# Performance work log

Measured on AMD Instinct MI355X. Metric: run time of the kernel, lower is better.

Reference implementation:

```python
import jax, jax.numpy as jnp
import numpy as np

S, B, E, H = 2048, 2, 1024, 16
DH = E // H
SCALING = DH ** -0.5


def setup_inputs() -> dict:
    key = jax.random.key(0)
    ks = jax.random.split(key, 9)
    std = 1.0 / np.sqrt(E)
    return {
        "query": jax.random.normal(ks[0], (S, B, E), jnp.float32),
        "wq": jax.random.normal(ks[1], (E, E), jnp.float32) * std,
        "bq": jax.random.normal(ks[2], (E,), jnp.float32) * 0.02,
        "wk": jax.random.normal(ks[3], (E, E), jnp.float32) * std,
        "bk": jax.random.normal(ks[4], (E,), jnp.float32) * 0.02,
        "wv": jax.random.normal(ks[5], (E, E), jnp.float32) * std,
        "bv": jax.random.normal(ks[6], (E,), jnp.float32) * 0.02,
        "wo": jax.random.normal(ks[7], (E, E), jnp.float32) * std,
        "bo": jax.random.normal(ks[8], (E,), jnp.float32) * 0.02,
    }


def reference(query, wq, bq, wk, bk, wv, bv, wo, bo):
    # query: [S, B, E] (time, batch, channel), self-attention: key=value=query
    q = (query @ wq.T + bq) * SCALING          # fairseq scales q, not scores
    k = query @ wk.T + bk
    v = query @ wv.T + bv
    # split heads: [S, B, H, DH]
    q = q.reshape(S, B, H, DH)
    k = k.reshape(S, B, H, DH)
    v = v.reshape(S, B, H, DH)
    scores = jnp.einsum("qbhd,kbhd->bhqk", q, k)   # [B, H, S, S]
    probs = jax.nn.softmax(scores, axis=-1)
    ctx = jnp.einsum("bhqk,kbhd->qbhd", probs, v)  # [S, B, H, DH]
    ctx = ctx.reshape(S, B, E)
    return ctx @ wo.T + bo                          # [S, B, E]
```

## Files before the change

### kernel.cpp

```cpp
#include <hip/hip_runtime.h>
#include <hip/hip_bf16.h>
#include <stdint.h>

#define S_LEN 2048
#define BATCH 2
#define EMB   1024
#define NH    16
#define DHEAD 64
#define ROWS  (S_LEN*BATCH)
#define SCALE_Q 0.18033688011112042f
#define DEFER_THR 11.0f

typedef __attribute__((ext_vector_type(8))) short bf16x8;
typedef __attribute__((ext_vector_type(4))) float f32x4;
typedef __attribute__((ext_vector_type(16))) float f32x16;

typedef const __attribute__((address_space(1))) void* gas_ptr;
typedef __attribute__((address_space(3))) void* las_ptr;
#define GLD16(g, l) __builtin_amdgcn_global_load_lds((gas_ptr)(g), (las_ptr)(l), 16, 0, 0)

__device__ __forceinline__ unsigned short f2b(float f) {
  union { float f; unsigned int u; } v; v.f = f;
  unsigned int u = v.u;
  unsigned int r = (u + 0x7FFFu + ((u >> 16) & 1u)) >> 16;
  return (unsigned short)r;
}

__device__ __forceinline__ unsigned cvt_pk_bf16(float lo, float hi) {
  unsigned r;
  asm("v_cvt_pk_bf16_f32 %0, %1, %2" : "=v"(r) : "v"(lo), "v"(hi));
  return r;
}

__device__ __forceinline__ float exp2_raw(float x) {
  float r;
  asm("v_exp_f32 %0, %1" : "=v"(r) : "v"(x));
  return r;
}

__device__ __forceinline__ void cvt8(const float* __restrict__ s,
                                     unsigned short* __restrict__ d, size_t i) {
  float4 a = *reinterpret_cast<const float4*>(s + i);
  float4 b = *reinterpret_cast<const float4*>(s + i + 4);
  uint4 o;
  o.x = (unsigned)f2b(a.x) | ((unsigned)f2b(a.y) << 16);
  o.y = (unsigned)f2b(a.z) | ((unsigned)f2b(a.w) << 16);
  o.z = (unsigned)f2b(b.x) | ((unsigned)f2b(b.y) << 16);
  o.w = (unsigned)f2b(b.z) | ((unsigned)f2b(b.w) << 16);
  *reinterpret_cast<uint4*>(d + i) = o;
}

__global__ __launch_bounds__(256) void cvt_all_kernel(
    const float* __restrict__ query,
    const float* __restrict__ wq, const float* __restrict__ wk,
    const float* __restrict__ wv, const float* __restrict__ wo,
    unsigned short* __restrict__ Xbf,
    unsigned short* __restrict__ Wqb, unsigned short* __restrict__ Wkb,
    unsigned short* __restrict__ Wvb, unsigned short* __restrict__ Wob) {
  int id = blockIdx.x;
  const float* s; unsigned short* d; size_t off;
  if (id < 2048) { s = query; d = Xbf; off = (size_t)id * 2048; }
  else {
    int wsel = (id - 2048) >> 9;
    off = (size_t)((id - 2048) & 511) * 2048;
    switch (wsel) {
      case 0:  s = wq; d = Wqb; break;
      case 1:  s = wk; d = Wkb; break;
      case 2:  s = wv; d = Wvb; break;
      default: s = wo; d = Wob; break;
    }
  }
  cvt8(s, d, off + (size_t)threadIdx.x * 8);
}

__device__ __forceinline__ void gemm_mainloop(const unsigned short* __restrict__ A,
                                              const unsigned short* __restrict__ Bw,
                                              int m0, int n0, f32x4 acc[4][4],
                                              unsigned short* Ab, unsigned short* Bb) {
  const int t    = threadIdx.x;
  const int lane = t & 63;
  const int w    = t >> 6;
  const int wr   = w >> 1, wc = w & 1;
  const int lm   = lane & 15;
  const int lq   = lane >> 4;

  f32x4 zf = {0.0f, 0.0f, 0.0f, 0.0f};
#pragma unroll
  for (int i = 0; i < 4; ++i)
#pragma unroll
    for (int j = 0; j < 4; ++j) acc[i][j] = zf;

  for (int k0 = 0; k0 < EMB; k0 += 64) {
#pragma unroll
    for (int q = 0; q < 4; ++q) {
      int c = t + q * 256;
      int r = c >> 3, ci = c & 7;
      int lc = ci ^ (r & 7);
      GLD16(A  + (size_t)(m0 + r) * EMB + k0 + lc * 8,
            (char*)Ab + (size_t)(q * 256 + w * 64) * 16);
      GLD16(Bw + (size_t)(n0 + r) * EMB + k0 + lc * 8,
            (char*)Bb + (size_t)(q * 256 + w * 64) * 16);
    }
    asm volatile("s_waitcnt vmcnt(0)" ::: "memory");
    __syncthreads();

#pragma unroll
    for (int kk = 0; kk < 2; ++kk) {
      bf16x8 af[4], bfr[4];
#pragma unroll
      for (int i = 0; i < 4; ++i) {
        int ra = wr * 64 + i * 16 + lm;
        af[i] = *reinterpret_cast<const bf16x8*>(
            &Ab[ra * 64 + ((kk * 4 + lq) ^ (ra & 7)) * 8]);
      }
#pragma unroll
      for (int j = 0; j < 4; ++j) {
        int rb = wc * 64 + j * 16 + lm;
        bfr[j] = *reinterpret_cast<const bf16x8*>(
            &Bb[rb * 64 + ((kk * 4 + lq) ^ (rb & 7)) * 8]);
      }
#pragma unroll
      for (int i = 0; i < 4; ++i)
#pragma unroll
        for (int j = 0; j < 4; ++j)
          acc[i][j] = __builtin_amdgcn_mfma_f32_16x16x32_bf16(af[i], bfr[j], acc[i][j], 0, 0, 0);
    }
    __syncthreads();
  }
}

__global__ __launch_bounds__(256) void gemm_qkv_kernel(
    const unsigned short* __restrict__ X,
    const unsigned short* __restrict__ Wq, const unsigned short* __restrict__ Wk,
    const unsigned short* __restrict__ Wv,
    const float* __restrict__ bq, const float* __restrict__ bk, const float* __restrict__ bv,
    unsigned short* __restrict__ Qb, unsigned short* __restrict__ Kb,
    unsigned short* __restrict__ Vtg) {
  __shared__ unsigned short SH[2][128 * 64];
  const int m0 = blockIdx.x * 128;
  const int n0 = blockIdx.y * 128;
  const int z  = blockIdx.z;
  const unsigned short* Bw = (z == 0) ? Wq : (z == 1) ? Wk : Wv;
  const float* bias        = (z == 0) ? bq : (z == 1) ? bk : bv;

  f32x4 acc[4][4];
  gemm_mainloop(X, Bw, m0, n0, acc, SH[0], SH[1]);

  const int t    = threadIdx.x;
  const int lane = t & 63;
  const int w    = t >> 6;
  const int wr   = w >> 1, wc = w & 1;
  const int lm   = lane & 15, lq = lane >> 4;

  if (z != 2) {
    unsigned short* Out = (z == 0) ? Qb : Kb;
    const float scale   = (z == 0) ? SCALE_Q : 1.0f;
#pragma unroll
    for (int j = 0; j < 4; ++j) {
      int col = n0 + wc * 64 + j * 16 + lm;
      int h = col >> 6, dd = col & 63;
      float bc = bias[col];
#pragma unroll
      for (int i = 0; i < 4; ++i) {
#pragma unroll
        for (int r = 0; r < 4; ++r) {
          int row = m0 + wr * 64 + i * 16 + lq * 4 + r;
          int s = row >> 1, b = row & 1;
          float v = (acc[i][j][r] + bc) * scale;
          Out[((size_t)(b * NH + h) * S_LEN + s) * DHEAD + dd] = f2b(v);
        }
      }
    }
  } else {
    unsigned short* T = &SH[0][0];
#pragma unroll
    for (int j = 0; j < 4; ++j) {
      int col = wc * 64 + j * 16 + lm;
      float bc = bias[n0 + col];
#pragma unroll
      for (int i = 0; i < 4; ++i) {
#pragma unroll
        for (int r = 0; r < 4; ++r) {
          int row = wr * 64 + i * 16 + lq * 4 + r;
          int idx = (row & 1) * 64 + (row >> 1);
          int chunk = idx >> 3, within = idx & 7;
          int pchunk = (chunk & 8) | ((chunk ^ col) & 7);
          T[col * 128 + pchunk * 8 + within] = f2b(acc[i][j][r] + bc);
        }
      }
    }
    __syncthreads();
#pragma unroll
    for (int itr = 0; itr < 8; ++itr) {
      int u = (t >> 3) + itr * 32;
      int col = u & 127, b = u >> 7;
      int c3 = t & 7;
      int pchunk = (b * 8) | ((c3 ^ col) & 7);
      bf16x8 vv = *reinterpret_cast<const bf16x8*>(&T[col * 128 + pchunk * 8]);
      int h = (n0 + col) >> 6, dd = (n0 + col) & 63;
      unsigned short* dst =
          Vtg + ((size_t)(b * NH + h) * DHEAD + dd) * S_LEN + (m0 >> 1);
      int p1 = ((c3 >> 1) << 4) | ((c3 & 1) << 2);
      union { bf16x8 v; uint4 u4; } cv; cv.v = vv;
      *reinterpret_cast<uint2*>(dst + p1)     = make_uint2(cv.u4.x, cv.u4.y);
      *reinterpret_cast<uint2*>(dst + p1 + 8) = make_uint2(cv.u4.z, cv.u4.w);
    }
  }
}

__global__ __launch_bounds__(256) void gemm_out_kernel(
    const unsigned short* __restrict__ Ctx, const unsigned short* __restrict__ Wo,
    const float* __restrict__ bo, float* __restrict__ Out) {
  __shared__ unsigned short Ab[64 * 64];
  __shared__ unsigned short Bb[128 * 64];
  const int m0 = blockIdx.x * 64;
  const int n0 = blockIdx.y * 128;
  const int t    = threadIdx.x;
  const int lane = t & 63;
  const int w    = t >> 6;
  const int wr   = w >> 1, wc = w & 1;
  const int lm   = lane & 15, lq = lane >> 4;

  f32x4 zf = {0.0f, 0.0f, 0.0f, 0.0f};
  f32x4 acc[2][4];
#pragma unroll
  for (int i = 0; i < 2; ++i)
#pragma unroll
    for (int j = 0; j < 4; ++j) acc[i][j] = zf;

  for (int k0 = 0; k0 < EMB; k0 += 64) {
#pragma unroll
    for (int q = 0; q < 2; ++q) {
      int c = t + q * 256;
      int r = c >> 3, ci = c & 7;
      int lc = ci ^ (r & 7);
      GLD16(Ctx + (size_t)(m0 + r) * EMB + k0 + lc * 8,
            (char*)Ab + (size_t)(q * 256 + w * 64) * 16);
    }
#pragma unroll
    for (int q = 0; q < 4; ++q) {
      int c = t + q * 256;
      int r = c >> 3, ci = c & 7;
      int lc = ci ^ (r & 7);
      GLD16(Wo + (size_t)(n0 + r) * EMB + k0 + lc * 8,
            (char*)Bb + (size_t)(q * 256 + w * 64) * 16);
    }
    asm volatile("s_waitcnt vmcnt(0)" ::: "memory");
    __syncthreads();

#pragma unroll
    for (int kk = 0; kk < 2; ++kk) {
      bf16x8 af[2], bfr[4];
#pragma unroll
      for (int i = 0; i < 2; ++i) {
        int ra = wr * 32 + i * 16 + lm;
        af[i] = *reinterpret_cast<const bf16x8*>(
            &Ab[ra * 64 + ((kk * 4 + lq) ^ (ra & 7)) * 8]);
      }
#pragma unroll
      for (int j = 0; j < 4; ++j) {
        int rb = wc * 64 + j * 16 + lm;
        bfr[j] = *reinterpret_cast<const bf16x8*>(
            &Bb[rb * 64 + ((kk * 4 + lq) ^ (rb & 7)) * 8]);
      }
#pragma unroll
      for (int i = 0; i < 2; ++i)
#pragma unroll
        for (int j = 0; j < 4; ++j)
          acc[i][j] = __builtin_amdgcn_mfma_f32_16x16x32_bf16(af[i], bfr[j], acc[i][j], 0, 0, 0);
    }
    __syncthreads();
  }

#pragma unroll
  for (int j = 0; j < 4; ++j) {
    int col = n0 + wc * 64 + j * 16 + lm;
    float bc = bo[col];
#pragma unroll
    for (int i = 0; i < 2; ++i) {
#pragma unroll
      for (int r = 0; r < 4; ++r) {
        int row = m0 + wr * 32 + i * 16 + lq * 4 + r;
        Out[(size_t)row * EMB + col] = acc[i][j][r] + bc;
      }
    }
  }
}

__global__ __launch_bounds__(256, 2) void attn_kernel(
    const unsigned short* __restrict__ Qb, const unsigned short* __restrict__ Kb,
    const unsigned short* __restrict__ Vtg, unsigned short* __restrict__ Ctx) {
  const int bh = blockIdx.x;
  const int q0 = blockIdx.y * 128;
  const int t    = threadIdx.x;
  const int lane = t & 63;
  const int w    = t >> 6;
  const int l31  = lane & 31;
  const int hh   = lane >> 5;
  const unsigned short* Q  = Qb  + (size_t)bh * S_LEN * DHEAD;
  const unsigned short* K  = Kb  + (size_t)bh * S_LEN * DHEAD;
  const unsigned short* Vt = Vtg + (size_t)bh * DHEAD * S_LEN;

  __shared__ unsigned short Kl[2][64 * 64];
  __shared__ unsigned short Vl[2][64 * 64];

  const int qw = q0 + w * 32;

  bf16x8 aq[4];
#pragma unroll
  for (int kk = 0; kk < 4; ++kk)
    aq[kk] = *reinterpret_cast<const bf16x8*>(
        Q + (size_t)(qw + l31) * DHEAD + kk * 16 + hh * 8);

  f32x16 z16 = {0.f,0.f,0.f,0.f, 0.f,0.f,0.f,0.f, 0.f,0.f,0.f,0.f, 0.f,0.f,0.f,0.f};
  f32x16 accO[2];
  accO[0] = z16; accO[1] = z16;
  float m_s = -1e30f, l_s = 0.0f;

  auto STAGE = [&](int b, int kb) {
#pragma unroll
    for (int q = 0; q < 2; ++q) {
      int c = t + q * 256;
      int r = c >> 3, p = c & 7;
      int lc = p ^ (r & 7);
      GLD16(K  + (size_t)(kb + r) * DHEAD + lc * 8,
            (char*)&Kl[b][0] + (size_t)(q * 256 + w * 64) * 16);
      GLD16(Vt + (size_t)r * S_LEN + kb + lc * 8,
            (char*)&Vl[b][0] + (size_t)(q * 256 + w * 64) * 16);
    }
  };

  const int NT = S_LEN / 64;
  STAGE(0, 0);
  STAGE(1, 64);

  for (int it = 0; it < NT; ++it) {
    const int cur = it & 1;
    if (it < NT - 1) {
      asm volatile("s_waitcnt vmcnt(4)" ::: "memory");
    } else {
      asm volatile("s_waitcnt vmcnt(0)" ::: "memory");
    }
    __builtin_amdgcn_s_barrier();

    f32x16 p32[2];
    __builtin_amdgcn_s_setprio(1);
#pragma unroll
    for (int ji = 0; ji < 2; ++ji) {
      f32x16 a = z16;
      int rr = ji * 32 + l31;
#pragma unroll
      for (int kk = 0; kk < 4; ++kk) {
        bf16x8 kf = *reinterpret_cast<const bf16x8*>(
            &Kl[cur][rr * 64 + ((kk * 2 + hh) ^ (rr & 7)) * 8]);
        a = __builtin_amdgcn_mfma_f32_32x32x16_bf16(kf, aq[kk], a, 0, 0, 0);
      }
      p32[ji] = a;
    }
    __builtin_amdgcn_s_setprio(0);

    float t8[8];
#pragma unroll
    for (int e = 0; e < 8; ++e)
      t8[e] = fmaxf(fmaxf(p32[0][e], p32[0][e + 8]),
                    fmaxf(p32[1][e], p32[1][e + 8]));
    float u0 = fmaxf(t8[0], t8[4]), u1 = fmaxf(t8[1], t8[5]);
    float u2 = fmaxf(t8[2], t8[6]), u3 = fmaxf(t8[3], t8[7]);
    float tm = fmaxf(fmaxf(u0, u1), fmaxf(u2, u3));
    tm = fmaxf(tm, __shfl_xor(tm, 32));

    if (!__all(tm - m_s <= DEFER_THR)) {
      float mn = fmaxf(m_s, tm);
      float sc = exp2_raw(m_s - mn);
      l_s *= sc;
      m_s = mn;
#pragma unroll
      for (int r = 0; r < 16; ++r) {
        float scr = __shfl(sc, (r & 3) + 8 * (r >> 2) + 4 * hh);
        accO[0][r] *= scr;
        accO[1][r] *= scr;
      }
    }

#pragma unroll
    for (int e = 0; e < 16; ++e) {
      p32[0][e] = exp2_raw(p32[0][e] - m_s);
      p32[1][e] = exp2_raw(p32[1][e] - m_s);
    }
    float s8[8];
#pragma unroll
    for (int e = 0; e < 8; ++e)
      s8[e] = (p32[0][e] + p32[0][e + 8]) + (p32[1][e] + p32[1][e + 8]);
    float v0 = (s8[0] + s8[4]) + (s8[1] + s8[5]);
    float v1 = (s8[2] + s8[6]) + (s8[3] + s8[7]);
    float ps = v0 + v1;
    ps += __shfl_xor(ps, 32);
    l_s += ps;

    bf16x8 pa[2][2];
#pragma unroll
    for (int ji = 0; ji < 2; ++ji) {
      uint4 lo4, hi4;
      lo4.x = cvt_pk_bf16(p32[ji][0],  p32[ji][1]);
      lo4.y = cvt_pk_bf16(p32[ji][2],  p32[ji][3]);
      lo4.z = cvt_pk_bf16(p32[ji][4],  p32[ji][5]);
      lo4.w = cvt_pk_bf16(p32[ji][6],  p32[ji][7]);
      hi4.x = cvt_pk_bf16(p32[ji][8],  p32[ji][9]);
      hi4.y = cvt_pk_bf16(p32[ji][10], p32[ji][11]);
      hi4.z = cvt_pk_bf16(p32[ji][12], p32[ji][13]);
      hi4.w = cvt_pk_bf16(p32[ji][14], p32[ji][15]);
      pa[ji][0] = *reinterpret_cast<bf16x8*>(&lo4);
      pa[ji][1] = *reinterpret_cast<bf16x8*>(&hi4);
    }

    __builtin_amdgcn_s_setprio(1);
#pragma unroll
    for (int ni = 0; ni < 2; ++ni) {
      int dd = ni * 32 + l31;
#pragma unroll
      for (int ji = 0; ji < 2; ++ji)
#pragma unroll
        for (int ss = 0; ss < 2; ++ss) {
          bf16x8 bv = *reinterpret_cast<const bf16x8*>(
              &Vl[cur][dd * 64 + ((ji * 4 + ss * 2 + hh) ^ (dd & 7)) * 8]);
          accO[ni] = __builtin_amdgcn_mfma_f32_32x32x16_bf16(pa[ji][ss], bv, accO[ni], 0, 0, 0);
        }
    }
    __builtin_amdgcn_s_setprio(0);

    asm volatile("s_waitcnt lgkmcnt(0)" ::: "memory");
    __builtin_amdgcn_sched_barrier(0);
    __builtin_amdgcn_s_barrier();

    if (it + 2 < NT) STAGE(cur, (it + 2) * 64);
  }

  const int b = bh >> 4, h = bh & 15;
#pragma unroll
  for (int r = 0; r < 16; ++r) {
    int row = (r & 3) + 8 * (r >> 2) + 4 * hh;
    float rl = 1.0f / __shfl(l_s, row);
    int srow = qw + row;
    size_t base = ((size_t)srow * BATCH + b) * EMB + (size_t)h * 64 + l31;
    Ctx[base]      = f2b(accO[0][r] * rl);
    Ctx[base + 32] = f2b(accO[1][r] * rl);
  }
}

extern "C" void kernel_launch(void* const* d_in, const int* in_sizes, int n_in,
                              void* d_out, int out_size, void* d_ws, size_t ws_size,
                              hipStream_t stream) {
  const float* query = (const float*)d_in[0];
  const float* wq = (const float*)d_in[1];
  const float* bq = (const float*)d_in[2];
  const float* wk = (const float*)d_in[3];
  const float* bk = (const float*)d_in[4];
  const float* wv = (const float*)d_in[5];
  const float* bv = (const float*)d_in[6];
  const float* wo = (const float*)d_in[7];
  const float* bo = (const float*)d_in[8];
  float* out = (float*)d_out;

  unsigned short* p = (unsigned short*)d_ws;
  unsigned short* Xbf = p;                        p += (size_t)ROWS * EMB;
  unsigned short* Wqb = p;                        p += (size_t)EMB * EMB;
  unsigned short* Wkb = p;                        p += (size_t)EMB * EMB;
  unsigned short* Wvb = p;                        p += (size_t)EMB * EMB;
  unsigned short* Wob = p;                        p += (size_t)EMB * EMB;
  unsigned short* Qb  = p;                        p += (size_t)ROWS * EMB;
  unsigned short* Kb  = p;                        p += (size_t)ROWS * EMB;
  unsigned short* Vtg = p;                        p += (size_t)ROWS * EMB;
  unsigned short* Ctx = p;                        p += (size_t)ROWS * EMB;

  cvt_all_kernel<<<4096, 256, 0, stream>>>(query, wq, wk, wv, wo,
                                           Xbf, Wqb, Wkb, Wvb, Wob);
  gemm_qkv_kernel<<<dim3(ROWS / 128, EMB / 128, 3), 256, 0, stream>>>(
      Xbf, Wqb, Wkb, Wvb, bq, bk, bv, Qb, Kb, Vtg);
  attn_kernel<<<dim3(BATCH * NH, S_LEN / 128), 256, 0, stream>>>(Qb, Kb, Vtg, Ctx);
  gemm_out_kernel<<<dim3(ROWS / 64, EMB / 128), 256, 0, stream>>>(Ctx, Wob, bo, out);
}
```

Before: 196.0 us.

## Load K/V fragments directly from global into registers, dropping LDS staging

```diff
diff --git a/kernel.cpp b/kernel.cpp
--- a/kernel.cpp
+++ b/kernel.cpp
@@ -287,7 +287,7 @@
   }
 }
 
-__global__ __launch_bounds__(256, 2) void attn_kernel(
+__global__ __launch_bounds__(256) void attn_kernel(
     const unsigned short* __restrict__ Qb, const unsigned short* __restrict__ Kb,
     const unsigned short* __restrict__ Vtg, unsigned short* __restrict__ Ctx) {
   const int bh = blockIdx.x;
@@ -301,9 +301,6 @@
   const unsigned short* K  = Kb  + (size_t)bh * S_LEN * DHEAD;
   const unsigned short* Vt = Vtg + (size_t)bh * DHEAD * S_LEN;
 
-  __shared__ unsigned short Kl[2][64 * 64];
-  __shared__ unsigned short Vl[2][64 * 64];
-
   const int qw = q0 + w * 32;
 
   bf16x8 aq[4];
@@ -317,122 +314,114 @@
   accO[0] = z16; accO[1] = z16;
   float m_s = -1e30f, l_s = 0.0f;
 
-  auto STAGE = [&](int b, int kb) {
-#pragma unroll
-    for (int q = 0; q < 2; ++q) {
-      int c = t + q * 256;
-      int r = c >> 3, p = c & 7;
-      int lc = p ^ (r & 7);
-      GLD16(K  + (size_t)(kb + r) * DHEAD + lc * 8,
-            (char*)&Kl[b][0] + (size_t)(q * 256 + w * 64) * 16);
-      GLD16(Vt + (size_t)r * S_LEN + kb + lc * 8,
-            (char*)&Vl[b][0] + (size_t)(q * 256 + w * 64) * 16);
-    }
-  };
+  bf16x8 kfA[2][4], kfB[2][4], bv[2][2][2];
+
+#define LOADK(KF, kb)                                                        \
+  {                                                                          \
+    _Pragma("unroll")                                                        \
+    for (int ji = 0; ji < 2; ++ji)                                           \
+      _Pragma("unroll")                                                      \
+      for (int kk = 0; kk < 4; ++kk)                                         \
+        KF[ji][kk] = *reinterpret_cast<const bf16x8*>(                       \
+            K + (size_t)((kb) + ji * 32 + l31) * DHEAD + kk * 16 + hh * 8);  \
+  }
+#define LOADV(kb)                                                            \
+  {                                                                          \
+    _Pragma("unroll")                                                        \
+    for (int ni = 0; ni < 2; ++ni)                                           \
+      _Pragma("unroll")                                                      \
+      for (int ji = 0; ji < 2; ++ji)                                         \
+        _Pragma("unroll")                                                    \
+        for (int ss = 0; ss < 2; ++ss)                                       \
+          bv[ni][ji][ss] = *reinterpret_cast<const bf16x8*>(                 \
+              Vt + (size_t)(ni * 32 + l31) * S_LEN + (kb) +                  \
+              (ji * 4 + ss * 2 + hh) * 8);                                   \
+  }
+
+#define COMPUTE(KF)                                                          \
+  {                                                                          \
+    f32x16 p32[2];                                                           \
+    __builtin_amdgcn_s_setprio(1);                                           \
+    _Pragma("unroll")                                                        \
+    for (int ji = 0; ji < 2; ++ji) {                                         \
+      f32x16 a = z16;                                                        \
+      _Pragma("unroll")                                                      \
+      for (int kk = 0; kk < 4; ++kk)                                         \
+        a = __builtin_amdgcn_mfma_f32_32x32x16_bf16(KF[ji][kk], aq[kk], a, 0, 0, 0); \
+      p32[ji] = a;                                                           \
+    }                                                                        \
+    __builtin_amdgcn_s_setprio(0);                                           \
+    float t8[8];                                                             \
+    _Pragma("unroll")                                                        \
+    for (int e = 0; e < 8; ++e)                                              \
+      t8[e] = fmaxf(fmaxf(p32[0][e], p32[0][e + 8]),                         \
+                    fmaxf(p32[1][e], p32[1][e + 8]));                        \
+    float u0 = fmaxf(t8[0], t8[4]), u1 = fmaxf(t8[1], t8[5]);                \
+    float u2 = fmaxf(t8[2], t8[6]), u3 = fmaxf(t8[3], t8[7]);                \
+    float tm = fmaxf(fmaxf(u0, u1), fmaxf(u2, u3));                          \
+    tm = fmaxf(tm, __shfl_xor(tm, 32));                                      \
+    if (!__all(tm - m_s <= DEFER_THR)) {                                     \
+      float mn = fmaxf(m_s, tm);                                             \
+      float sc = exp2_raw(m_s - mn);                                         \
+      l_s *= sc;                                                             \
+      m_s = mn;                                                              \
+      _Pragma("unroll")                                                      \
+      for (int r = 0; r < 16; ++r) {                                         \
+        float scr = __shfl(sc, (r & 3) + 8 * (r >> 2) + 4 * hh);             \
+        accO[0][r] *= scr;                                                   \
+        accO[1][r] *= scr;                                                   \
+      }                                                                      \
+    }                                                                        \
+    _Pragma("unroll")                                                        \
+    for (int e = 0; e < 16; ++e) {                                           \
+      p32[0][e] = exp2_raw(p32[0][e] - m_s);                                 \
+      p32[1][e] = exp2_raw(p32[1][e] - m_s);                                 \
+    }                                                                        \
+    float s8[8];                                                             \
+    _Pragma("unroll")                                                        \
+    for (int e = 0; e < 8; ++e)                                              \
+      s8[e] = (p32[0][e] + p32[0][e + 8]) + (p32[1][e] + p32[1][e + 8]);     \
+    float v0 = (s8[0] + s8[4]) + (s8[1] + s8[5]);                            \
+    float v1 = (s8[2] + s8[6]) + (s8[3] + s8[7]);                            \
+    float ps = v0 + v1;                                                      \
+    ps += __shfl_xor(ps, 32);                                                \
+    l_s += ps;                                                               \
+    bf16x8 pa[2][2];                                                         \
+    _Pragma("unroll")                                                        \
+    for (int ji = 0; ji < 2; ++ji) {                                         \
+      uint4 lo4, hi4;                                                        \
+      lo4.x = cvt_pk_bf16(p32[ji][0],  p32[ji][1]);                          \
+      lo4.y = cvt_pk_bf16(p32[ji][2],  p32[ji][3]);                          \
+      lo4.z = cvt_pk_bf16(p32[ji][4],  p32[ji][5]);                          \
+      lo4.w = cvt_pk_bf16(p32[ji][6],  p32[ji][7]);                          \
+      hi4.x = cvt_pk_bf16(p32[ji][8],  p32[ji][9]);                          \
+      hi4.y = cvt_pk_bf16(p32[ji][10], p32[ji][11]);                         \
+      hi4.z = cvt_pk_bf16(p32[ji][12], p32[ji][13]);                         \
+      hi4.w = cvt_pk_bf16(p32[ji][14], p32[ji][15]);                         \
+      pa[ji][0] = *reinterpret_cast<bf16x8*>(&lo4);                          \
+      pa[ji][1] = *reinterpret_cast<bf16x8*>(&hi4);                          \
+    }                                                                        \
+    __builtin_amdgcn_s_setprio(1);                                           \
+    _Pragma("unroll")                                                        \
+    for (int ni = 0; ni < 2; ++ni)                                           \
+      _Pragma("unroll")                                                      \
+      for (int ji = 0; ji < 2; ++ji)                                         \
+        _Pragma("unroll")                                                    \
+        for (int ss = 0; ss < 2; ++ss)                                       \
+          accO[ni] = __builtin_amdgcn_mfma_f32_32x32x16_bf16(                \
+              pa[ji][ss], bv[ni][ji][ss], accO[ni], 0, 0, 0);                \
+    __builtin_amdgcn_s_setprio(0);                                           \
+  }
 
   const int NT = S_LEN / 64;
-  STAGE(0, 0);
-  STAGE(1, 64);
-
-  for (int it = 0; it < NT; ++it) {
-    const int cur = it & 1;
-    if (it < NT - 1) {
-      asm volatile("s_waitcnt vmcnt(4)" ::: "memory");
-    } else {
-      asm volatile("s_waitcnt vmcnt(0)" ::: "memory");
-    }
-    __builtin_amdgcn_s_barrier();
-
-    f32x16 p32[2];
-    __builtin_amdgcn_s_setprio(1);
-#pragma unroll
-    for (int ji = 0; ji < 2; ++ji) {
-      f32x16 a = z16;
-      int rr = ji * 32 + l31;
-#pragma unroll
-      for (int kk = 0; kk < 4; ++kk) {
-        bf16x8 kf = *reinterpret_cast<const bf16x8*>(
-            &Kl[cur][rr * 64 + ((kk * 2 + hh) ^ (rr & 7)) * 8]);
-        a = __builtin_amdgcn_mfma_f32_32x32x16_bf16(kf, aq[kk], a, 0, 0, 0);
-      }
-      p32[ji] = a;
-    }
-    __builtin_amdgcn_s_setprio(0);
-
-    float t8[8];
-#pragma unroll
-    for (int e = 0; e < 8; ++e)
-      t8[e] = fmaxf(fmaxf(p32[0][e], p32[0][e + 8]),
-                    fmaxf(p32[1][e], p32[1][e + 8]));
-    float u0 = fmaxf(t8[0], t8[4]), u1 = fmaxf(t8[1], t8[5]);
-    float u2 = fmaxf(t8[2], t8[6]), u3 = fmaxf(t8[3], t8[7]);
-    float tm = fmaxf(fmaxf(u0, u1), fmaxf(u2, u3));
-    tm = fmaxf(tm, __shfl_xor(tm, 32));
-
-    if (!__all(tm - m_s <= DEFER_THR)) {
-      float mn = fmaxf(m_s, tm);
-      float sc = exp2_raw(m_s - mn);
-      l_s *= sc;
-      m_s = mn;
-#pragma unroll
-      for (int r = 0; r < 16; ++r) {
-        float scr = __shfl(sc, (r & 3) + 8 * (r >> 2) + 4 * hh);
-        accO[0][r] *= scr;
-        accO[1][r] *= scr;
-      }
-    }
-
-#pragma unroll
-    for (int e = 0; e < 16; ++e) {
-      p32[0][e] = exp2_raw(p32[0][e] - m_s);
-      p32[1][e] = exp2_raw(p32[1][e] - m_s);
-    }
-    float s8[8];
-#pragma unroll
-    for (int e = 0; e < 8; ++e)
-      s8[e] = (p32[0][e] + p32[0][e + 8]) + (p32[1][e] + p32[1][e + 8]);
-    float v0 = (s8[0] + s8[4]) + (s8[1] + s8[5]);
-    float v1 = (s8[2] + s8[6]) + (s8[3] + s8[7]);
-    float ps = v0 + v1;
-    ps += __shfl_xor(ps, 32);
-    l_s += ps;
-
-    bf16x8 pa[2][2];
-#pragma unroll
-    for (int ji = 0; ji < 2; ++ji) {
-      uint4 lo4, hi4;
-      lo4.x = cvt_pk_bf16(p32[ji][0],  p32[ji][1]);
-      lo4.y = cvt_pk_bf16(p32[ji][2],  p32[ji][3]);
-      lo4.z = cvt_pk_bf16(p32[ji][4],  p32[ji][5]);
-      lo4.w = cvt_pk_bf16(p32[ji][6],  p32[ji][7]);
-      hi4.x = cvt_pk_bf16(p32[ji][8],  p32[ji][9]);
-      hi4.y = cvt_pk_bf16(p32[ji][10], p32[ji][11]);
-      hi4.z = cvt_pk_bf16(p32[ji][12], p32[ji][13]);
-      hi4.w = cvt_pk_bf16(p32[ji][14], p32[ji][15]);
-      pa[ji][0] = *reinterpret_cast<bf16x8*>(&lo4);
-      pa[ji][1] = *reinterpret_cast<bf16x8*>(&hi4);
-    }
-
-    __builtin_amdgcn_s_setprio(1);
-#pragma unroll
-    for (int ni = 0; ni < 2; ++ni) {
-      int dd = ni * 32 + l31;
-#pragma unroll
-      for (int ji = 0; ji < 2; ++ji)
-#pragma unroll
-        for (int ss = 0; ss < 2; ++ss) {
-          bf16x8 bv = *reinterpret_cast<const bf16x8*>(
-              &Vl[cur][dd * 64 + ((ji * 4 + ss * 2 + hh) ^ (dd & 7)) * 8]);
-          accO[ni] = __builtin_amdgcn_mfma_f32_32x32x16_bf16(pa[ji][ss], bv, accO[ni], 0, 0, 0);
-        }
-    }
-    __builtin_amdgcn_s_setprio(0);
-
-    asm volatile("s_waitcnt lgkmcnt(0)" ::: "memory");
-    __builtin_amdgcn_sched_barrier(0);
-    __builtin_amdgcn_s_barrier();
-
-    if (it + 2 < NT) STAGE(cur, (it + 2) * 64);
+  LOADK(kfA, 0);
+  for (int it = 0; it < NT; it += 2) {
+    LOADK(kfB, (it + 1) * 64);
+    LOADV(it * 64);
+    COMPUTE(kfA);
+    if (it + 2 < NT) LOADK(kfA, (it + 2) * 64);
+    LOADV((it + 1) * 64);
+    COMPUTE(kfB);
   }
 
   const int b = bh >> 4, h = bh & 15;
```

Result: slower. 265.3 us (+35.4%).

## Split KV range across two wave groups per block and merge in LDS

Applied to the files above, without the earlier changes.

```diff
diff --git a/kernel.cpp b/kernel.cpp
--- a/kernel.cpp
+++ b/kernel.cpp
@@ -287,7 +287,7 @@
   }
 }
 
-__global__ __launch_bounds__(256, 2) void attn_kernel(
+__global__ __launch_bounds__(512, 4) void attn_kernel(
     const unsigned short* __restrict__ Qb, const unsigned short* __restrict__ Kb,
     const unsigned short* __restrict__ Vtg, unsigned short* __restrict__ Ctx) {
   const int bh = blockIdx.x;
@@ -295,16 +295,20 @@
   const int t    = threadIdx.x;
   const int lane = t & 63;
   const int w    = t >> 6;
+  const int hf   = w >> 2;
+  const int wl   = w & 3;
+  const int th   = t & 255;
   const int l31  = lane & 31;
   const int hh   = lane >> 5;
   const unsigned short* Q  = Qb  + (size_t)bh * S_LEN * DHEAD;
   const unsigned short* K  = Kb  + (size_t)bh * S_LEN * DHEAD;
   const unsigned short* Vt = Vtg + (size_t)bh * DHEAD * S_LEN;
 
-  __shared__ unsigned short Kl[2][64 * 64];
-  __shared__ unsigned short Vl[2][64 * 64];
-
-  const int qw = q0 + w * 32;
+  alignas(16) __shared__ char SMEM[65536];
+  unsigned short* Kl = (unsigned short*)(SMEM + hf * 32768);
+  unsigned short* Vl = (unsigned short*)(SMEM + hf * 32768 + 16384);
+
+  const int qw = q0 + wl * 32;
 
   bf16x8 aq[4];
 #pragma unroll
@@ -320,19 +324,20 @@
   auto STAGE = [&](int b, int kb) {
 #pragma unroll
     for (int q = 0; q < 2; ++q) {
-      int c = t + q * 256;
-      int r = c >> 3, p = c & 7;
-      int lc = p ^ (r & 7);
-      GLD16(K  + (size_t)(kb + r) * DHEAD + lc * 8,
-            (char*)&Kl[b][0] + (size_t)(q * 256 + w * 64) * 16);
+      int c = th + q * 256;
+      int r = c >> 3, pp = c & 7;
+      int lc = pp ^ (r & 7);
+      GLD16(K + (size_t)(kb + r) * DHEAD + lc * 8,
+            (char*)Kl + (size_t)b * 8192 + (size_t)(q * 256 + wl * 64) * 16);
       GLD16(Vt + (size_t)r * S_LEN + kb + lc * 8,
-            (char*)&Vl[b][0] + (size_t)(q * 256 + w * 64) * 16);
+            (char*)Vl + (size_t)b * 8192 + (size_t)(q * 256 + wl * 64) * 16);
     }
   };
 
-  const int NT = S_LEN / 64;
-  STAGE(0, 0);
-  STAGE(1, 64);
+  const int kvbase = hf * (S_LEN / 2);
+  const int NT = S_LEN / 2 / 64;
+  STAGE(0, kvbase);
+  STAGE(1, kvbase + 64);
 
   for (int it = 0; it < NT; ++it) {
     const int cur = it & 1;
@@ -343,6 +348,9 @@
     }
     __builtin_amdgcn_s_barrier();
 
+    const unsigned short* Klc = Kl + cur * 4096;
+    const unsigned short* Vlc = Vl + cur * 4096;
+
     f32x16 p32[2];
     __builtin_amdgcn_s_setprio(1);
 #pragma unroll
@@ -352,7 +360,7 @@
 #pragma unroll
       for (int kk = 0; kk < 4; ++kk) {
         bf16x8 kf = *reinterpret_cast<const bf16x8*>(
-            &Kl[cur][rr * 64 + ((kk * 2 + hh) ^ (rr & 7)) * 8]);
+            &Klc[rr * 64 + ((kk * 2 + hh) ^ (rr & 7)) * 8]);
         a = __builtin_amdgcn_mfma_f32_32x32x16_bf16(kf, aq[kk], a, 0, 0, 0);
       }
       p32[ji] = a;
@@ -422,7 +430,7 @@
 #pragma unroll
         for (int ss = 0; ss < 2; ++ss) {
           bf16x8 bv = *reinterpret_cast<const bf16x8*>(
-              &Vl[cur][dd * 64 + ((ji * 4 + ss * 2 + hh) ^ (dd & 7)) * 8]);
+              &Vlc[dd * 64 + ((ji * 4 + ss * 2 + hh) ^ (dd & 7)) * 8]);
           accO[ni] = __builtin_amdgcn_mfma_f32_32x32x16_bf16(pa[ji][ss], bv, accO[ni], 0, 0, 0);
         }
     }
@@ -432,18 +440,42 @@
     __builtin_amdgcn_sched_barrier(0);
     __builtin_amdgcn_s_barrier();
 
-    if (it + 2 < NT) STAGE(cur, (it + 2) * 64);
-  }
-
-  const int b = bh >> 4, h = bh & 15;
-#pragma unroll
-  for (int r = 0; r < 16; ++r) {
-    int row = (r & 3) + 8 * (r >> 2) + 4 * hh;
-    float rl = 1.0f / __shfl(l_s, row);
-    int srow = qw + row;
-    size_t base = ((size_t)srow * BATCH + b) * EMB + (size_t)h * 64 + l31;
-    Ctx[base]      = f2b(accO[0][r] * rl);
-    Ctx[base + 32] = f2b(accO[1][r] * rl);
+    if (it + 2 < NT) STAGE(cur, kvbase + (it + 2) * 64);
+  }
+
+  float* MB = (float*)SMEM;
+  const int MS = 35;
+  const int mb = (wl * 64 + lane) * MS;
+  if (hf == 1) {
+    MB[mb]     = m_s;
+    MB[mb + 1] = l_s;
+#pragma unroll
+    for (int r = 0; r < 16; ++r) {
+      MB[mb + 2 + r]  = accO[0][r];
+      MB[mb + 18 + r] = accO[1][r];
+    }
+  }
+  __syncthreads();
+  if (hf == 0) {
+    float m1 = MB[mb], l1 = MB[mb + 1];
+    float mn  = fmaxf(m_s, m1);
+    float sc0 = exp2_raw(m_s - mn);
+    float sc1 = exp2_raw(m1 - mn);
+    float lf  = l_s * sc0 + l1 * sc1;
+    const int b = bh >> 4, h = bh & 15;
+#pragma unroll
+    for (int r = 0; r < 16; ++r) {
+      int row = (r & 3) + 8 * (r >> 2) + 4 * hh;
+      float s0 = __shfl(sc0, row);
+      float s1 = __shfl(sc1, row);
+      float rl = 1.0f / __shfl(lf, row);
+      float o0 = (accO[0][r] * s0 + MB[mb + 2 + r]  * s1) * rl;
+      float o1 = (accO[1][r] * s0 + MB[mb + 18 + r] * s1) * rl;
+      int srow = qw + row;
+      size_t base = ((size_t)srow * BATCH + b) * EMB + (size_t)h * 64 + l31;
+      Ctx[base]      = f2b(o0);
+      Ctx[base + 32] = f2b(o1);
+    }
   }
 }
 
@@ -476,6 +508,6 @@
                                            Xbf, Wqb, Wkb, Wvb, Wob);
   gemm_qkv_kernel<<<dim3(ROWS / 128, EMB / 128, 3), 256, 0, stream>>>(
       Xbf, Wqb, Wkb, Wvb, bq, bk, bv, Qb, Kb, Vtg);
-  attn_kernel<<<dim3(BATCH * NH, S_LEN / 128), 256, 0, stream>>>(Qb, Kb, Vtg, Ctx);
+  attn_kernel<<<dim3(BATCH * NH, S_LEN / 128), 512, 0, stream>>>(Qb, Kb, Vtg, Ctx);
   gemm_out_kernel<<<dim3(ROWS / 64, EMB / 128), 256, 0, stream>>>(Ctx, Wob, bo, out);
 }
```

Result: no change. 194.9 us (-0.5%).
